# Performance work log

Hardware: AMD Instinct MI355X
Metric: run time of the kernel (lower is better)

The kernel has to match this reference:

```python
import jax, jax.numpy as jnp
import numpy as np

N_NODES = 100000
N_EDGES = 1600000


def setup_inputs() -> dict:
    key = jax.random.key(0)
    ks = jax.random.split(key, 5)
    x = jax.random.normal(ks[0], (N_NODES, 128), dtype=jnp.float32)
    edge_index = jax.random.randint(ks[1], (2, N_EDGES), 0, N_NODES, dtype=jnp.int64)
    edge_weight = jnp.ones((N_EDGES,), dtype=jnp.float32)
    W1 = jax.random.normal(ks[2], (128, 128), dtype=jnp.float32) * (1.0 / np.sqrt(128))
    b1 = jnp.zeros((128,), dtype=jnp.float32)
    W2 = jax.random.normal(ks[3], (128, 64), dtype=jnp.float32) * (1.0 / np.sqrt(128))
    b2 = jnp.zeros((64,), dtype=jnp.float32)
    return {"x": x, "edge_index": edge_index, "edge_weight": edge_weight,
            "W1": W1, "b1": b1, "W2": W2, "b2": b2}


def _gcn_conv(x, rows, cols, W, b, n_nodes):
    # GCNConv(normalize=True), unit edge weights (forward overwrites weights with ones)
    h = x @ W                                             # [N, out]
    ones_w = jnp.ones(rows.shape[0], dtype=x.dtype)
    deg = jax.ops.segment_sum(ones_w, cols, num_segments=n_nodes)   # in-degree at targets
    dinv = jnp.where(deg > 0, deg ** -0.5, 0.0)
    norm = dinv[rows] * dinv[cols]                        # [E+N]
    msg = h[rows] * norm[:, None]                         # gather + scale, memory-bound
    out = jax.ops.segment_sum(msg, cols, num_segments=n_nodes)
    return out + b


def reference(x, edge_index, edge_weight, W1, b1, W2, b2):
    n = x.shape[0]
    loop = jnp.arange(n, dtype=edge_index.dtype)
    rows = jnp.concatenate([edge_index[0], loop])         # self-loops (PyG default)
    cols = jnp.concatenate([edge_index[1], loop])
    h = jax.nn.relu(_gcn_conv(x, rows, cols, W1, b1, n))
    logits = _gcn_conv(h, rows, cols, W2, b2, n)
    return logits
```

## Files before the change

kernel.cpp:

```cpp
#include <hip/hip_runtime.h>
#include <hip/hip_fp16.h>


constexpr int NN = 100000;
constexpr int NE = 1600000;
constexpr int BSH = 7;
constexpr int NB = (NN + 127) >> BSH;
constexpr int NBLK = 256;
constexpr int EPB = NE / NBLK;
constexpr int TSTR = 784;

typedef _Float16 f16x8 __attribute__((ext_vector_type(8)));
typedef float f32x4 __attribute__((ext_vector_type(4)));

__global__ __launch_bounds__(256) void k_hist(const int* __restrict__ cols,
                                              int* __restrict__ table) {
  __shared__ int cnt[NB];
  for (int i = threadIdx.x; i < NB; i += 256) cnt[i] = 0;
  __syncthreads();
  int base = blockIdx.x * EPB;
  for (int i = threadIdx.x; i < EPB; i += 256)
    atomicAdd(&cnt[cols[base + i] >> BSH], 1);
  __syncthreads();
  for (int i = threadIdx.x; i < NB; i += 256)
    table[blockIdx.x * TSTR + i] = cnt[i];
}

__global__ __launch_bounds__(256) void k_scanT(const int* __restrict__ table,
                                               int* __restrict__ startOff,
                                               int* __restrict__ btot) {
  __shared__ int s[256];
  int b = blockIdx.x, t = threadIdx.x;
  int v = table[t * TSTR + b];
  s[t] = v;
  __syncthreads();
  for (int off = 1; off < 256; off <<= 1) {
    int tmp = (t >= off) ? s[t - off] : 0;
    __syncthreads();
    s[t] += tmp;
    __syncthreads();
  }
  startOff[t * TSTR + b] = s[t] - v;
  if (t == 255) btot[b] = s[t];
}

__global__ __launch_bounds__(256) void k_scanBkt(const int* __restrict__ btot,
                                                 int* __restrict__ bucketBase) {
  __shared__ int s[256];
  int t = threadIdx.x;
  int base = t * 4;
  int d0 = (base + 0 < NB) ? btot[base + 0] : 0;
  int d1 = (base + 1 < NB) ? btot[base + 1] : 0;
  int d2 = (base + 2 < NB) ? btot[base + 2] : 0;
  int d3 = (base + 3 < NB) ? btot[base + 3] : 0;
  int tsum = d0 + d1 + d2 + d3;
  s[t] = tsum;
  __syncthreads();
  for (int off = 1; off < 256; off <<= 1) {
    int tmp = (t >= off) ? s[t - off] : 0;
    __syncthreads();
    s[t] += tmp;
    __syncthreads();
  }
  int ex = s[t] - tsum;
  if (base + 0 < NB) bucketBase[base + 0] = ex;
  if (base + 1 < NB) bucketBase[base + 1] = ex + d0;
  if (base + 2 < NB) bucketBase[base + 2] = ex + d0 + d1;
  if (base + 3 < NB) bucketBase[base + 3] = ex + d0 + d1 + d2;
}

__global__ __launch_bounds__(256) void k_scat(const int* __restrict__ rows,
                                              const int* __restrict__ cols,
                                              const int* __restrict__ startOff,
                                              const int* __restrict__ bucketBase,
                                              unsigned* __restrict__ binned) {
  __shared__ int scnt[NB];
  int blk = blockIdx.x;
  for (int i = threadIdx.x; i < NB; i += 256)
    scnt[i] = bucketBase[i] + startOff[blk * TSTR + i];
  __syncthreads();
  int base = blk * EPB;
  for (int i = threadIdx.x; i < EPB; i += 256) {
    int c = cols[base + i];
    int r = rows[base + i];
    int pos = atomicAdd(&scnt[c >> BSH], 1);
    binned[pos] = ((unsigned)r << BSH) | (unsigned)(c & 127);
  }
}

__global__ __launch_bounds__(256) void k_fillb(const unsigned* __restrict__ binned,
                                               const int* __restrict__ bucketBase,
                                               const int* __restrict__ btot,
                                               int* __restrict__ rowptr,
                                               int* __restrict__ deg,
                                               float* __restrict__ dinv,
                                               int* __restrict__ srcIdx,
                                               const float4* __restrict__ x4,
                                               float2* __restrict__ y8) {
  __shared__ int cnt[128];
  __shared__ int sc[128];
  __shared__ int rp[128];
  __shared__ float sdv[128];
  int b = blockIdx.x;
  int nb0 = b << BSH;
  int nn = min(128, NN - nb0);
  int tid = threadIdx.x;
  if (tid < 128) cnt[tid] = 0;
  __syncthreads();
  int ebeg = bucketBase[b];
  int eend = ebeg + btot[b];
  for (int p = ebeg + tid; p < eend; p += 256)
    atomicAdd(&cnt[binned[p] & 127], 1);
  __syncthreads();
  int v = (tid < 128) ? cnt[tid] : 0;
  if (tid < 128) sc[tid] = v;
  __syncthreads();
  for (int off = 1; off < 128; off <<= 1) {
    int tmp = (tid < 128 && tid >= off) ? sc[tid - off] : 0;
    __syncthreads();
    if (tid < 128) sc[tid] += tmp;
    __syncthreads();
  }
  if (tid < 128) {
    int ex = sc[tid] - v;
    rp[tid] = ebeg + ex;
    float dv = rsqrtf((float)v + 1.0f);
    sdv[tid] = dv;
    if (tid < nn) {
      rowptr[nb0 + tid] = ebeg + ex;
      deg[nb0 + tid] = v;
      dinv[nb0 + tid] = dv;
    }
    cnt[tid] = 0;
  }
  __syncthreads();
  for (int p = ebeg + tid; p < eend; p += 256) {
    unsigned pk = binned[p];
    int cl = pk & 127;
    int local = atomicAdd(&cnt[cl], 1);
    srcIdx[rp[cl] + local] = (int)(pk >> BSH);
  }
  int tot = nn << 5;
  const float4* xb = x4 + ((size_t)nb0 << 5);
  float2* yb = y8 + ((size_t)nb0 << 5);
  for (int i = tid; i < tot; i += 256) {
    float s = sdv[i >> 5];
    float4 vv = xb[i];
    union { __half2 h[2]; float2 f; } u;
    u.h[0] = __floats2half2_rn(vv.x * s, vv.y * s);
    u.h[1] = __floats2half2_rn(vv.z * s, vv.w * s);
    yb[i] = u.f;
  }
}

__global__ __launch_bounds__(256) void k_wt(const float* __restrict__ W1,
                                            const float* __restrict__ W2,
                                            __half* __restrict__ Wt1,
                                            __half* __restrict__ Wt2) {
  int i = blockIdx.x * 256 + threadIdx.x;
  if (i < 16384) {
    int k = i >> 7, n = i & 127;
    Wt1[n * 128 + k] = __float2half(W1[i]);
  } else {
    int j = i - 16384;
    int k = j >> 6, n = j & 63;
    Wt2[n * 128 + k] = __float2half(W2[j]);
  }
}

__global__ __launch_bounds__(256, 8) void k_fused(
    const __half* __restrict__ y, const int* __restrict__ rowptr,
    const int* __restrict__ deg, const int* __restrict__ srcIdx,
    const float* __restrict__ dinv, const __half* __restrict__ Wt1,
    const float* __restrict__ b1, const __half* __restrict__ Wt2,
    __half* __restrict__ z) {
  __shared__ __align__(16) __half sA[16][136];
  __shared__ __align__(16) __half sB[16][136];
  const int w = threadIdx.x >> 6, l = threadIdx.x & 63;
  const int blk0 = blockIdx.x * 16;
  const int quad = l >> 4, m = l & 15;

  for (int i = 0; i < 4; ++i) {
    const int lr = w * 4 + i;
    const int node = blk0 + lr;
    const int d = deg[node];
    const int ptr = rowptr[node];
    float acc[8];
#pragma unroll
    for (int j = 0; j < 8; j++) acc[j] = 0.0f;
    for (int base = 0; base < d; base += 64) {
      int cnt = min(64, d - base);
      int my = (l < cnt) ? srcIdx[ptr + base + l] : 0;
      int k = 0;
      for (; k + 16 <= cnt; k += 16) {
        int s0 = __shfl(my, k + quad);
        int s1 = __shfl(my, k + 4 + quad);
        int s2 = __shfl(my, k + 8 + quad);
        int s3 = __shfl(my, k + 12 + quad);
        f16x8 v0 = *reinterpret_cast<const f16x8*>(y + (size_t)s0 * 128 + m * 8);
        f16x8 v1 = *reinterpret_cast<const f16x8*>(y + (size_t)s1 * 128 + m * 8);
        f16x8 v2 = *reinterpret_cast<const f16x8*>(y + (size_t)s2 * 128 + m * 8);
        f16x8 v3 = *reinterpret_cast<const f16x8*>(y + (size_t)s3 * 128 + m * 8);
#pragma unroll
        for (int j = 0; j < 8; j++) acc[j] += (float)v0[j];
#pragma unroll
        for (int j = 0; j < 8; j++) acc[j] += (float)v1[j];
#pragma unroll
        for (int j = 0; j < 8; j++) acc[j] += (float)v2[j];
#pragma unroll
        for (int j = 0; j < 8; j++) acc[j] += (float)v3[j];
      }
      for (; k + 8 <= cnt; k += 8) {
        int s0 = __shfl(my, k + quad);
        int s1 = __shfl(my, k + 4 + quad);
        f16x8 v0 = *reinterpret_cast<const f16x8*>(y + (size_t)s0 * 128 + m * 8);
        f16x8 v1 = *reinterpret_cast<const f16x8*>(y + (size_t)s1 * 128 + m * 8);
#pragma unroll
        for (int j = 0; j < 8; j++) acc[j] += (float)v0[j];
#pragma unroll
        for (int j = 0; j < 8; j++) acc[j] += (float)v1[j];
      }
      for (; k < cnt; k += 4) {
        int idx = k + quad;
        bool valid = idx < cnt;
        int s0 = __shfl(my, valid ? idx : 0);
        f16x8 v0 = *reinterpret_cast<const f16x8*>(y + (size_t)s0 * 128 + m * 8);
        if (valid) {
#pragma unroll
          for (int j = 0; j < 8; j++) acc[j] += (float)v0[j];
        }
      }
    }
#pragma unroll
    for (int j = 0; j < 8; j++) acc[j] += __shfl_xor(acc[j], 16);
#pragma unroll
    for (int j = 0; j < 8; j++) acc[j] += __shfl_xor(acc[j], 32);
    if (quad == 0) {
      f16x8 sv = *reinterpret_cast<const f16x8*>(y + (size_t)node * 128 + m * 8);
      float scn = dinv[node];
      f16x8 o;
#pragma unroll
      for (int j = 0; j < 8; j++)
        o[j] = (_Float16)((acc[j] + (float)sv[j]) * scn);
      *reinterpret_cast<f16x8*>(&sA[lr][m * 8]) = o;
    }
  }
  __syncthreads();

  f16x8 afrag[4];
#pragma unroll
  for (int kk = 0; kk < 4; kk++)
    afrag[kk] = *reinterpret_cast<const f16x8*>(&sA[m][kk * 32 + quad * 8]);
  f32x4 acc1[2];
#pragma unroll
  for (int t = 0; t < 2; t++) {
    float bv = b1[(w * 2 + t) * 16 + m];
    acc1[t] = (f32x4){bv, bv, bv, bv};
  }
#pragma unroll
  for (int kk = 0; kk < 4; kk++) {
#pragma unroll
    for (int t = 0; t < 2; t++) {
      f16x8 b = *reinterpret_cast<const f16x8*>(
          Wt1 + (size_t)((w * 2 + t) * 16 + m) * 128 + kk * 32 + quad * 8);
      acc1[t] = __builtin_amdgcn_mfma_f32_16x16x32_f16(afrag[kk], b, acc1[t], 0, 0, 0);
    }
  }
#pragma unroll
  for (int t = 0; t < 2; t++)
#pragma unroll
    for (int i = 0; i < 4; i++)
      sB[quad * 4 + i][(w * 2 + t) * 16 + m] =
          __float2half(fmaxf(acc1[t][i], 0.0f));
  __syncthreads();

  f16x8 hfrag[4];
#pragma unroll
  for (int kk = 0; kk < 4; kk++)
    hfrag[kk] = *reinterpret_cast<const f16x8*>(&sB[m][kk * 32 + quad * 8]);
  f32x4 acc2 = (f32x4){0.f, 0.f, 0.f, 0.f};
#pragma unroll
  for (int kk = 0; kk < 4; kk++) {
    f16x8 b = *reinterpret_cast<const f16x8*>(
        Wt2 + (size_t)(w * 16 + m) * 128 + kk * 32 + quad * 8);
    acc2 = __builtin_amdgcn_mfma_f32_16x16x32_f16(hfrag[kk], b, acc2, 0, 0, 0);
  }
  float rs[4];
#pragma unroll
  for (int i = 0; i < 4; i++) rs[i] = dinv[blk0 + quad * 4 + i];
#pragma unroll
  for (int i = 0; i < 4; i++)
    sA[quad * 4 + i][w * 16 + m] = __float2half(acc2[i] * rs[i]);
  __syncthreads();

  if (threadIdx.x < 128) {
    int r = threadIdx.x >> 3, cc = threadIdx.x & 7;
    *reinterpret_cast<float4*>(z + (size_t)(blk0 + r) * 64 + cc * 8) =
        *reinterpret_cast<const float4*>(&sA[r][cc * 8]);
  }
}

__global__ __launch_bounds__(256) void k_gath2(const __half* __restrict__ z,
                                               const int* __restrict__ rowptr,
                                               const int* __restrict__ deg,
                                               const int* __restrict__ srcIdx,
                                               const float* __restrict__ dinv,
                                               const float* __restrict__ b2,
                                               float* __restrict__ out) {
  int node = blockIdx.x * 4 + (threadIdx.x >> 6);
  if (node >= NN) return;
  int lane = threadIdx.x & 63;
  int g = lane >> 3;
  int c = lane & 7;
  int d = deg[node];
  int p = rowptr[node];
  size_t coff = (size_t)c * 8;
  float acc[8];
#pragma unroll
  for (int i = 0; i < 8; i++) acc[i] = 0.0f;

  for (int base = 0; base < d; base += 64) {
    int cnt = min(64, d - base);
    int my = (lane < cnt) ? srcIdx[p + base + lane] : 0;
    int k = 0;
    for (; k + 16 <= cnt; k += 16) {
      int s0 = __shfl(my, k + g);
      int s1 = __shfl(my, k + 8 + g);
      f16x8 v0 = *reinterpret_cast<const f16x8*>(z + (size_t)s0 * 64 + coff);
      f16x8 v1 = *reinterpret_cast<const f16x8*>(z + (size_t)s1 * 64 + coff);
#pragma unroll
      for (int i = 0; i < 8; i++) acc[i] += (float)v0[i];
#pragma unroll
      for (int i = 0; i < 8; i++) acc[i] += (float)v1[i];
    }
    for (; k < cnt; k += 8) {
      int idx = k + g;
      bool valid = idx < cnt;
      int s0 = __shfl(my, valid ? idx : 0);
      f16x8 v0 = *reinterpret_cast<const f16x8*>(z + (size_t)s0 * 64 + coff);
      if (valid) {
#pragma unroll
        for (int i = 0; i < 8; i++) acc[i] += (float)v0[i];
      }
    }
  }
#pragma unroll
  for (int i = 0; i < 8; i++) acc[i] += __shfl_xor(acc[i], 8);
#pragma unroll
  for (int i = 0; i < 8; i++) acc[i] += __shfl_xor(acc[i], 16);
#pragma unroll
  for (int i = 0; i < 8; i++) acc[i] += __shfl_xor(acc[i], 32);
  if (g == 0) {
    f16x8 sv = *reinterpret_cast<const f16x8*>(z + (size_t)node * 64 + coff);
    float s = dinv[node];
    const float4* b4 = reinterpret_cast<const float4*>(b2);
    float4 bv0 = b4[2 * c], bv1 = b4[2 * c + 1];
    float4 o0, o1;
    o0.x = (acc[0] + (float)sv[0]) * s + bv0.x;
    o0.y = (acc[1] + (float)sv[1]) * s + bv0.y;
    o0.z = (acc[2] + (float)sv[2]) * s + bv0.z;
    o0.w = (acc[3] + (float)sv[3]) * s + bv0.w;
    o1.x = (acc[4] + (float)sv[4]) * s + bv1.x;
    o1.y = (acc[5] + (float)sv[5]) * s + bv1.y;
    o1.z = (acc[6] + (float)sv[6]) * s + bv1.z;
    o1.w = (acc[7] + (float)sv[7]) * s + bv1.w;
    float4* op = reinterpret_cast<float4*>(out + (size_t)node * 64 + coff);
    op[0] = o0;
    op[1] = o1;
  }
}

extern "C" void kernel_launch(void* const* d_in, const int* in_sizes, int n_in,
                              void* d_out, int out_size, void* d_ws, size_t ws_size,
                              hipStream_t stream) {
  const float* x  = (const float*)d_in[0];
  const int*   ei = (const int*)d_in[1];
  const int* rows = ei;
  const int* cols = ei + NE;
  const float* W1 = (const float*)d_in[3];
  const float* b1 = (const float*)d_in[4];
  const float* W2 = (const float*)d_in[5];
  const float* b2 = (const float*)d_in[6];
  float* out = (float*)d_out;

  char* base = (char*)d_ws;
  constexpr size_t MB = 1 << 20;
  int*      deg       = (int*)(base + 0 * MB);
  int*      rowptr    = (int*)(base + 1 * MB);
  float*    dinv      = (float*)(base + 2 * MB);
  int*      btot      = (int*)(base + 3 * MB);
  int*      bucketBase= (int*)(base + 3 * MB + 16 * 1024);
  __half*   Wt1       = (__half*)(base + 3 * MB + 64 * 1024);
  __half*   Wt2       = (__half*)(base + 3 * MB + 128 * 1024);
  int*      table     = (int*)(base + 4 * MB);
  int*      startOff  = (int*)(base + 5 * MB);
  unsigned* binned    = (unsigned*)(base + 6 * MB);
  int*      srcIdx    = (int*)(base + 13 * MB);
  __half*   y         = (__half*)(base + 20 * MB);
  __half*   z         = (__half*)(base + 46 * MB);

  k_wt<<<96, 256, 0, stream>>>(W1, W2, Wt1, Wt2);
  k_hist<<<NBLK, 256, 0, stream>>>(cols, table);
  k_scanT<<<NB, 256, 0, stream>>>(table, startOff, btot);
  k_scanBkt<<<1, 256, 0, stream>>>(btot, bucketBase);
  k_scat<<<NBLK, 256, 0, stream>>>(rows, cols, startOff, bucketBase, binned);
  k_fillb<<<NB, 256, 0, stream>>>(binned, bucketBase, btot, rowptr, deg, dinv,
                                  srcIdx, (const float4*)x, (float2*)y);
  k_fused<<<NN / 16, 256, 0, stream>>>(y, rowptr, deg, srcIdx, dinv,
                                       Wt1, b1, Wt2, z);
  k_gath2<<<(NN + 3) / 4, 256, 0, stream>>>(z, rowptr, deg, srcIdx, dinv, b2, out);
}
```

Before: 302.2 us.

## Merge all GCN stages into one persistent kernel with grid barriers

Replaces the eight separate kernel launches (histogram, scans, scatter, CSR fill, fused layer-1 GEMM, layer-2 gather) with a single persistent cooperative-style kernel. Grid-wide atomic barriers separate the phases, and the final gather uses an atomic work counter for dynamic load balancing. The aim is to remove launch overhead and inter-kernel gaps. In exchange it adds spin-wait barrier cost, relies on every block being co-resident for correctness, and leaves fewer blocks resident for the memory-bound gather phases.

```diff
diff --git a/kernel.cpp b/kernel.cpp
--- a/kernel.cpp
+++ b/kernel.cpp
@@ -9,372 +9,405 @@
 constexpr int NBLK = 256;
 constexpr int EPB = NE / NBLK;
 constexpr int TSTR = 784;
+constexpr int NTILE = NN / 16;
+constexpr int NG4 = NN / 4;
 
 typedef _Float16 f16x8 __attribute__((ext_vector_type(8)));
 typedef float f32x4 __attribute__((ext_vector_type(4)));
 
-__global__ __launch_bounds__(256) void k_hist(const int* __restrict__ cols,
-                                              int* __restrict__ table) {
-  __shared__ int cnt[NB];
-  for (int i = threadIdx.x; i < NB; i += 256) cnt[i] = 0;
+__device__ __forceinline__ void gsync(int* cnt, int* gen, int& local) {
   __syncthreads();
-  int base = blockIdx.x * EPB;
-  for (int i = threadIdx.x; i < EPB; i += 256)
-    atomicAdd(&cnt[cols[base + i] >> BSH], 1);
+  if (threadIdx.x == 0) {
+    int a = __hip_atomic_fetch_add(cnt, 1, __ATOMIC_ACQ_REL,
+                                   __HIP_MEMORY_SCOPE_AGENT);
+    if (a == (int)gridDim.x - 1) {
+      __hip_atomic_store(cnt, 0, __ATOMIC_RELAXED, __HIP_MEMORY_SCOPE_AGENT);
+      __hip_atomic_fetch_add(gen, 1, __ATOMIC_ACQ_REL,
+                             __HIP_MEMORY_SCOPE_AGENT);
+    } else {
+      while (__hip_atomic_load(gen, __ATOMIC_RELAXED,
+                               __HIP_MEMORY_SCOPE_SYSTEM) < local + 1)
+        __builtin_amdgcn_s_sleep(2);
+      (void)__hip_atomic_load(gen, __ATOMIC_ACQUIRE, __HIP_MEMORY_SCOPE_AGENT);
+    }
+  }
+  local++;
   __syncthreads();
-  for (int i = threadIdx.x; i < NB; i += 256)
-    table[blockIdx.x * TSTR + i] = cnt[i];
 }
 
-__global__ __launch_bounds__(256) void k_scanT(const int* __restrict__ table,
-                                               int* __restrict__ startOff,
-                                               int* __restrict__ btot) {
-  __shared__ int s[256];
-  int b = blockIdx.x, t = threadIdx.x;
-  int v = table[t * TSTR + b];
-  s[t] = v;
-  __syncthreads();
-  for (int off = 1; off < 256; off <<= 1) {
-    int tmp = (t >= off) ? s[t - off] : 0;
-    __syncthreads();
-    s[t] += tmp;
-    __syncthreads();
-  }
-  startOff[t * TSTR + b] = s[t] - v;
-  if (t == 255) btot[b] = s[t];
-}
-
-__global__ __launch_bounds__(256) void k_scanBkt(const int* __restrict__ btot,
-                                                 int* __restrict__ bucketBase) {
-  __shared__ int s[256];
-  int t = threadIdx.x;
-  int base = t * 4;
-  int d0 = (base + 0 < NB) ? btot[base + 0] : 0;
-  int d1 = (base + 1 < NB) ? btot[base + 1] : 0;
-  int d2 = (base + 2 < NB) ? btot[base + 2] : 0;
-  int d3 = (base + 3 < NB) ? btot[base + 3] : 0;
-  int tsum = d0 + d1 + d2 + d3;
-  s[t] = tsum;
-  __syncthreads();
-  for (int off = 1; off < 256; off <<= 1) {
-    int tmp = (t >= off) ? s[t - off] : 0;
-    __syncthreads();
-    s[t] += tmp;
-    __syncthreads();
-  }
-  int ex = s[t] - tsum;
-  if (base + 0 < NB) bucketBase[base + 0] = ex;
-  if (base + 1 < NB) bucketBase[base + 1] = ex + d0;
-  if (base + 2 < NB) bucketBase[base + 2] = ex + d0 + d1;
-  if (base + 3 < NB) bucketBase[base + 3] = ex + d0 + d1 + d2;
-}
-
-__global__ __launch_bounds__(256) void k_scat(const int* __restrict__ rows,
-                                              const int* __restrict__ cols,
-                                              const int* __restrict__ startOff,
-                                              const int* __restrict__ bucketBase,
-                                              unsigned* __restrict__ binned) {
-  __shared__ int scnt[NB];
-  int blk = blockIdx.x;
-  for (int i = threadIdx.x; i < NB; i += 256)
-    scnt[i] = bucketBase[i] + startOff[blk * TSTR + i];
-  __syncthreads();
-  int base = blk * EPB;
-  for (int i = threadIdx.x; i < EPB; i += 256) {
-    int c = cols[base + i];
-    int r = rows[base + i];
-    int pos = atomicAdd(&scnt[c >> BSH], 1);
-    binned[pos] = ((unsigned)r << BSH) | (unsigned)(c & 127);
-  }
-}
-
-__global__ __launch_bounds__(256) void k_fillb(const unsigned* __restrict__ binned,
-                                               const int* __restrict__ bucketBase,
-                                               const int* __restrict__ btot,
-                                               int* __restrict__ rowptr,
-                                               int* __restrict__ deg,
-                                               float* __restrict__ dinv,
-                                               int* __restrict__ srcIdx,
-                                               const float4* __restrict__ x4,
-                                               float2* __restrict__ y8) {
-  __shared__ int cnt[128];
-  __shared__ int sc[128];
-  __shared__ int rp[128];
-  __shared__ float sdv[128];
-  int b = blockIdx.x;
-  int nb0 = b << BSH;
-  int nn = min(128, NN - nb0);
-  int tid = threadIdx.x;
-  if (tid < 128) cnt[tid] = 0;
-  __syncthreads();
-  int ebeg = bucketBase[b];
-  int eend = ebeg + btot[b];
-  for (int p = ebeg + tid; p < eend; p += 256)
-    atomicAdd(&cnt[binned[p] & 127], 1);
-  __syncthreads();
-  int v = (tid < 128) ? cnt[tid] : 0;
-  if (tid < 128) sc[tid] = v;
-  __syncthreads();
-  for (int off = 1; off < 128; off <<= 1) {
-    int tmp = (tid < 128 && tid >= off) ? sc[tid - off] : 0;
-    __syncthreads();
-    if (tid < 128) sc[tid] += tmp;
-    __syncthreads();
-  }
-  if (tid < 128) {
-    int ex = sc[tid] - v;
-    rp[tid] = ebeg + ex;
-    float dv = rsqrtf((float)v + 1.0f);
-    sdv[tid] = dv;
-    if (tid < nn) {
-      rowptr[nb0 + tid] = ebeg + ex;
-      deg[nb0 + tid] = v;
-      dinv[nb0 + tid] = dv;
-    }
-    cnt[tid] = 0;
-  }
-  __syncthreads();
-  for (int p = ebeg + tid; p < eend; p += 256) {
-    unsigned pk = binned[p];
-    int cl = pk & 127;
-    int local = atomicAdd(&cnt[cl], 1);
-    srcIdx[rp[cl] + local] = (int)(pk >> BSH);
-  }
-  int tot = nn << 5;
-  const float4* xb = x4 + ((size_t)nb0 << 5);
-  float2* yb = y8 + ((size_t)nb0 << 5);
-  for (int i = tid; i < tot; i += 256) {
-    float s = sdv[i >> 5];
-    float4 vv = xb[i];
-    union { __half2 h[2]; float2 f; } u;
-    u.h[0] = __floats2half2_rn(vv.x * s, vv.y * s);
-    u.h[1] = __floats2half2_rn(vv.z * s, vv.w * s);
-    yb[i] = u.f;
-  }
-}
-
-__global__ __launch_bounds__(256) void k_wt(const float* __restrict__ W1,
-                                            const float* __restrict__ W2,
-                                            __half* __restrict__ Wt1,
-                                            __half* __restrict__ Wt2) {
-  int i = blockIdx.x * 256 + threadIdx.x;
-  if (i < 16384) {
-    int k = i >> 7, n = i & 127;
-    Wt1[n * 128 + k] = __float2half(W1[i]);
-  } else {
-    int j = i - 16384;
-    int k = j >> 6, n = j & 63;
-    Wt2[n * 128 + k] = __float2half(W2[j]);
-  }
-}
-
-__global__ __launch_bounds__(256, 8) void k_fused(
-    const __half* __restrict__ y, const int* __restrict__ rowptr,
-    const int* __restrict__ deg, const int* __restrict__ srcIdx,
-    const float* __restrict__ dinv, const __half* __restrict__ Wt1,
-    const float* __restrict__ b1, const __half* __restrict__ Wt2,
-    __half* __restrict__ z) {
-  __shared__ __align__(16) __half sA[16][136];
-  __shared__ __align__(16) __half sB[16][136];
-  const int w = threadIdx.x >> 6, l = threadIdx.x & 63;
-  const int blk0 = blockIdx.x * 16;
-  const int quad = l >> 4, m = l & 15;
-
-  for (int i = 0; i < 4; ++i) {
-    const int lr = w * 4 + i;
-    const int node = blk0 + lr;
-    const int d = deg[node];
-    const int ptr = rowptr[node];
-    float acc[8];
-#pragma unroll
-    for (int j = 0; j < 8; j++) acc[j] = 0.0f;
-    for (int base = 0; base < d; base += 64) {
-      int cnt = min(64, d - base);
-      int my = (l < cnt) ? srcIdx[ptr + base + l] : 0;
-      int k = 0;
-      for (; k + 16 <= cnt; k += 16) {
-        int s0 = __shfl(my, k + quad);
-        int s1 = __shfl(my, k + 4 + quad);
-        int s2 = __shfl(my, k + 8 + quad);
-        int s3 = __shfl(my, k + 12 + quad);
-        f16x8 v0 = *reinterpret_cast<const f16x8*>(y + (size_t)s0 * 128 + m * 8);
-        f16x8 v1 = *reinterpret_cast<const f16x8*>(y + (size_t)s1 * 128 + m * 8);
-        f16x8 v2 = *reinterpret_cast<const f16x8*>(y + (size_t)s2 * 128 + m * 8);
-        f16x8 v3 = *reinterpret_cast<const f16x8*>(y + (size_t)s3 * 128 + m * 8);
-#pragma unroll
-        for (int j = 0; j < 8; j++) acc[j] += (float)v0[j];
-#pragma unroll
-        for (int j = 0; j < 8; j++) acc[j] += (float)v1[j];
-#pragma unroll
-        for (int j = 0; j < 8; j++) acc[j] += (float)v2[j];
-#pragma unroll
-        for (int j = 0; j < 8; j++) acc[j] += (float)v3[j];
+__global__ __launch_bounds__(256, 8) void k_mega(
+    const float4* __restrict__ x4, const int* __restrict__ rows,
+    const int* __restrict__ cols, const float* __restrict__ W1,
+    const float* __restrict__ b1, const float* __restrict__ W2,
+    const float* __restrict__ b2, float* __restrict__ out,
+    int* __restrict__ table, int* __restrict__ startOff,
+    int* __restrict__ btot, int* __restrict__ bucketBase,
+    unsigned* __restrict__ binned, int* __restrict__ rowptr,
+    int* __restrict__ deg, float* __restrict__ dinv,
+    int* __restrict__ srcIdx, __half* __restrict__ Wt1,
+    __half* __restrict__ Wt2, __half* __restrict__ y,
+    __half* __restrict__ z, int* ctl) {
+  __shared__ __align__(16) char smem[8704];
+  __shared__ int sclaim;
+  const int tid = threadIdx.x;
+  const int nb_ = gridDim.x;
+  int* bcnt = ctl + 0;
+  int* bgen = ctl + 1;
+  int local = 0;
+
+  for (int vb = blockIdx.x; vb < NBLK + 96; vb += nb_) {
+    if (vb < NBLK) {
+      int* cnt = (int*)smem;
+      for (int i = tid; i < NB; i += 256) cnt[i] = 0;
+      __syncthreads();
+      int base = vb * EPB;
+      for (int i = tid; i < EPB; i += 256)
+        atomicAdd(&cnt[cols[base + i] >> BSH], 1);
+      __syncthreads();
+      for (int i = tid; i < NB; i += 256) table[vb * TSTR + i] = cnt[i];
+      __syncthreads();
+    } else {
+      int i = (vb - NBLK) * 256 + tid;
+      if (i < 16384) {
+        int k = i >> 7, n = i & 127;
+        Wt1[n * 128 + k] = __float2half(W1[i]);
+      } else {
+        int j = i - 16384;
+        int k = j >> 6, n = j & 63;
+        Wt2[n * 128 + k] = __float2half(W2[j]);
       }
-      for (; k + 8 <= cnt; k += 8) {
-        int s0 = __shfl(my, k + quad);
-        int s1 = __shfl(my, k + 4 + quad);
-        f16x8 v0 = *reinterpret_cast<const f16x8*>(y + (size_t)s0 * 128 + m * 8);
-        f16x8 v1 = *reinterpret_cast<const f16x8*>(y + (size_t)s1 * 128 + m * 8);
-#pragma unroll
-        for (int j = 0; j < 8; j++) acc[j] += (float)v0[j];
-#pragma unroll
-        for (int j = 0; j < 8; j++) acc[j] += (float)v1[j];
+    }
+  }
+  gsync(bcnt, bgen, local);
+
+  for (int vb = blockIdx.x; vb < NB; vb += nb_) {
+    int* s = (int*)smem;
+    int v = table[tid * TSTR + vb];
+    s[tid] = v;
+    __syncthreads();
+    for (int off = 1; off < 256; off <<= 1) {
+      int tmp = (tid >= off) ? s[tid - off] : 0;
+      __syncthreads();
+      s[tid] += tmp;
+      __syncthreads();
+    }
+    startOff[tid * TSTR + vb] = s[tid] - v;
+    if (tid == 255) btot[vb] = s[tid];
+    __syncthreads();
+  }
+  gsync(bcnt, bgen, local);
+
+  if (blockIdx.x < NBLK) {
+    int* bb = (int*)smem;
+    int* s = (int*)(smem + 3200);
+    int* scnt = (int*)(smem + 4352);
+    int base4 = tid * 4;
+    int d0 = (base4 + 0 < NB) ? btot[base4 + 0] : 0;
+    int d1 = (base4 + 1 < NB) ? btot[base4 + 1] : 0;
+    int d2 = (base4 + 2 < NB) ? btot[base4 + 2] : 0;
+    int d3 = (base4 + 3 < NB) ? btot[base4 + 3] : 0;
+    int tsum = d0 + d1 + d2 + d3;
+    s[tid] = tsum;
+    __syncthreads();
+    for (int off = 1; off < 256; off <<= 1) {
+      int tmp = (tid >= off) ? s[tid - off] : 0;
+      __syncthreads();
+      s[tid] += tmp;
+      __syncthreads();
+    }
+    int ex = s[tid] - tsum;
+    if (base4 + 0 < NB) bb[base4 + 0] = ex;
+    if (base4 + 1 < NB) bb[base4 + 1] = ex + d0;
+    if (base4 + 2 < NB) bb[base4 + 2] = ex + d0 + d1;
+    if (base4 + 3 < NB) bb[base4 + 3] = ex + d0 + d1 + d2;
+    __syncthreads();
+    if (blockIdx.x == 0)
+      for (int i = tid; i < NB; i += 256) bucketBase[i] = bb[i];
+    for (int vb = blockIdx.x; vb < NBLK; vb += nb_) {
+      for (int i = tid; i < NB; i += 256)
+        scnt[i] = bb[i] + startOff[vb * TSTR + i];
+      __syncthreads();
+      int base = vb * EPB;
+      for (int i = tid; i < EPB; i += 256) {
+        int c = cols[base + i];
+        int r = rows[base + i];
+        int pos = atomicAdd(&scnt[c >> BSH], 1);
+        binned[pos] = ((unsigned)r << BSH) | (unsigned)(c & 127);
       }
-      for (; k < cnt; k += 4) {
-        int idx = k + quad;
-        bool valid = idx < cnt;
-        int s0 = __shfl(my, valid ? idx : 0);
-        f16x8 v0 = *reinterpret_cast<const f16x8*>(y + (size_t)s0 * 128 + m * 8);
-        if (valid) {
-#pragma unroll
-          for (int j = 0; j < 8; j++) acc[j] += (float)v0[j];
-        }
+      __syncthreads();
+    }
+  }
+  gsync(bcnt, bgen, local);
+
+  for (int vb = blockIdx.x; vb < NB; vb += nb_) {
+    int* cnt = (int*)smem;
+    int* sc = cnt + 128;
+    int* rp = sc + 128;
+    int nb0 = vb << BSH;
+    int nn = min(128, NN - nb0);
+    if (tid < 128) cnt[tid] = 0;
+    __syncthreads();
+    int ebeg = bucketBase[vb];
+    int eend = ebeg + btot[vb];
+    for (int p = ebeg + tid; p < eend; p += 256)
+      atomicAdd(&cnt[binned[p] & 127], 1);
+    __syncthreads();
+    int v = (tid < 128) ? cnt[tid] : 0;
+    if (tid < 128) sc[tid] = v;
+    __syncthreads();
+    for (int off = 1; off < 128; off <<= 1) {
+      int tmp = (tid < 128 && tid >= off) ? sc[tid - off] : 0;
+      __syncthreads();
+      if (tid < 128) sc[tid] += tmp;
+      __syncthreads();
+    }
+    if (tid < 128) {
+      int ex = sc[tid] - v;
+      rp[tid] = ebeg + ex;
+      if (tid < nn) {
+        rowptr[nb0 + tid] = ebeg + ex;
+        deg[nb0 + tid] = v;
+        dinv[nb0 + tid] = rsqrtf((float)v + 1.0f);
       }
-    }
-#pragma unroll
-    for (int j = 0; j < 8; j++) acc[j] += __shfl_xor(acc[j], 16);
-#pragma unroll
-    for (int j = 0; j < 8; j++) acc[j] += __shfl_xor(acc[j], 32);
-    if (quad == 0) {
-      f16x8 sv = *reinterpret_cast<const f16x8*>(y + (size_t)node * 128 + m * 8);
-      float scn = dinv[node];
-      f16x8 o;
-#pragma unroll
-      for (int j = 0; j < 8; j++)
-        o[j] = (_Float16)((acc[j] + (float)sv[j]) * scn);
-      *reinterpret_cast<f16x8*>(&sA[lr][m * 8]) = o;
-    }
-  }
-  __syncthreads();
-
-  f16x8 afrag[4];
-#pragma unroll
-  for (int kk = 0; kk < 4; kk++)
-    afrag[kk] = *reinterpret_cast<const f16x8*>(&sA[m][kk * 32 + quad * 8]);
-  f32x4 acc1[2];
-#pragma unroll
-  for (int t = 0; t < 2; t++) {
-    float bv = b1[(w * 2 + t) * 16 + m];
-    acc1[t] = (f32x4){bv, bv, bv, bv};
-  }
-#pragma unroll
-  for (int kk = 0; kk < 4; kk++) {
-#pragma unroll
-    for (int t = 0; t < 2; t++) {
-      f16x8 b = *reinterpret_cast<const f16x8*>(
-          Wt1 + (size_t)((w * 2 + t) * 16 + m) * 128 + kk * 32 + quad * 8);
-      acc1[t] = __builtin_amdgcn_mfma_f32_16x16x32_f16(afrag[kk], b, acc1[t], 0, 0, 0);
-    }
-  }
-#pragma unroll
-  for (int t = 0; t < 2; t++)
-#pragma unroll
-    for (int i = 0; i < 4; i++)
-      sB[quad * 4 + i][(w * 2 + t) * 16 + m] =
-          __float2half(fmaxf(acc1[t][i], 0.0f));
-  __syncthreads();
-
-  f16x8 hfrag[4];
-#pragma unroll
-  for (int kk = 0; kk < 4; kk++)
-    hfrag[kk] = *reinterpret_cast<const f16x8*>(&sB[m][kk * 32 + quad * 8]);
-  f32x4 acc2 = (f32x4){0.f, 0.f, 0.f, 0.f};
-#pragma unroll
-  for (int kk = 0; kk < 4; kk++) {
-    f16x8 b = *reinterpret_cast<const f16x8*>(
-        Wt2 + (size_t)(w * 16 + m) * 128 + kk * 32 + quad * 8);
-    acc2 = __builtin_amdgcn_mfma_f32_16x16x32_f16(hfrag[kk], b, acc2, 0, 0, 0);
-  }
-  float rs[4];
-#pragma unroll
-  for (int i = 0; i < 4; i++) rs[i] = dinv[blk0 + quad * 4 + i];
-#pragma unroll
-  for (int i = 0; i < 4; i++)
-    sA[quad * 4 + i][w * 16 + m] = __float2half(acc2[i] * rs[i]);
-  __syncthreads();
-
-  if (threadIdx.x < 128) {
-    int r = threadIdx.x >> 3, cc = threadIdx.x & 7;
-    *reinterpret_cast<float4*>(z + (size_t)(blk0 + r) * 64 + cc * 8) =
-        *reinterpret_cast<const float4*>(&sA[r][cc * 8]);
-  }
-}
-
-__global__ __launch_bounds__(256) void k_gath2(const __half* __restrict__ z,
-                                               const int* __restrict__ rowptr,
-                                               const int* __restrict__ deg,
-                                               const int* __restrict__ srcIdx,
-                                               const float* __restrict__ dinv,
-                                               const float* __restrict__ b2,
-                                               float* __restrict__ out) {
-  int node = blockIdx.x * 4 + (threadIdx.x >> 6);
-  if (node >= NN) return;
-  int lane = threadIdx.x & 63;
-  int g = lane >> 3;
-  int c = lane & 7;
-  int d = deg[node];
-  int p = rowptr[node];
-  size_t coff = (size_t)c * 8;
-  float acc[8];
-#pragma unroll
-  for (int i = 0; i < 8; i++) acc[i] = 0.0f;
-
-  for (int base = 0; base < d; base += 64) {
-    int cnt = min(64, d - base);
-    int my = (lane < cnt) ? srcIdx[p + base + lane] : 0;
-    int k = 0;
-    for (; k + 16 <= cnt; k += 16) {
-      int s0 = __shfl(my, k + g);
-      int s1 = __shfl(my, k + 8 + g);
-      f16x8 v0 = *reinterpret_cast<const f16x8*>(z + (size_t)s0 * 64 + coff);
-      f16x8 v1 = *reinterpret_cast<const f16x8*>(z + (size_t)s1 * 64 + coff);
-#pragma unroll
-      for (int i = 0; i < 8; i++) acc[i] += (float)v0[i];
-#pragma unroll
-      for (int i = 0; i < 8; i++) acc[i] += (float)v1[i];
-    }
-    for (; k < cnt; k += 8) {
-      int idx = k + g;
-      bool valid = idx < cnt;
-      int s0 = __shfl(my, valid ? idx : 0);
-      f16x8 v0 = *reinterpret_cast<const f16x8*>(z + (size_t)s0 * 64 + coff);
-      if (valid) {
-#pragma unroll
-        for (int i = 0; i < 8; i++) acc[i] += (float)v0[i];
+      cnt[tid] = 0;
+    }
+    __syncthreads();
+    for (int p = ebeg + tid; p < eend; p += 256) {
+      unsigned pk = binned[p];
+      int cl = pk & 127;
+      int lo = atomicAdd(&cnt[cl], 1);
+      srcIdx[rp[cl] + lo] = (int)(pk >> BSH);
+    }
+    __syncthreads();
+  }
+  gsync(bcnt, bgen, local);
+
+  {
+    float2* y8 = (float2*)y;
+    for (int i = blockIdx.x * 256 + tid; i < NN * 32; i += nb_ * 256) {
+      float sfac = dinv[i >> 5];
+      float4 vv = x4[i];
+      union { __half2 h[2]; float2 f; } u;
+      u.h[0] = __floats2half2_rn(vv.x * sfac, vv.y * sfac);
+      u.h[1] = __floats2half2_rn(vv.z * sfac, vv.w * sfac);
+      y8[i] = u.f;
+    }
+  }
+  gsync(bcnt, bgen, local);
+
+  {
+    __half(*sA)[136] = (__half(*)[136])smem;
+    __half(*sB)[136] = (__half(*)[136])(smem + 4352);
+    const int w = tid >> 6, l = tid & 63;
+    const int quad = l >> 4, m = l & 15;
+    for (;;) {
+      if (tid == 0) sclaim = atomicAdd(ctl + 2, 1);
+      __syncthreads();
+      const int t0 = sclaim * 2;
+      if (t0 >= NTILE) break;
+      const int t1 = (t0 + 2 < NTILE) ? t0 + 2 : NTILE;
+      for (int tile = t0; tile < t1; ++tile) {
+        const int blk0 = tile * 16;
+        for (int i = 0; i < 4; ++i) {
+          const int lr = w * 4 + i;
+          const int node = blk0 + lr;
+          const int d = deg[node];
+          const int ptr = rowptr[node];
+          float acc[8];
+#pragma unroll
+          for (int j = 0; j < 8; j++) acc[j] = 0.0f;
+          for (int base = 0; base < d; base += 64) {
+            int cntv = min(64, d - base);
+            int my = (l < cntv) ? srcIdx[ptr + base + l] : 0;
+            int k = 0;
+            for (; k + 16 <= cntv; k += 16) {
+              int s0 = __shfl(my, k + quad);
+              int s1 = __shfl(my, k + 4 + quad);
+              int s2 = __shfl(my, k + 8 + quad);
+              int s3 = __shfl(my, k + 12 + quad);
+              f16x8 v0 = *(const f16x8*)(y + (size_t)s0 * 128 + m * 8);
+              f16x8 v1 = *(const f16x8*)(y + (size_t)s1 * 128 + m * 8);
+              f16x8 v2 = *(const f16x8*)(y + (size_t)s2 * 128 + m * 8);
+              f16x8 v3 = *(const f16x8*)(y + (size_t)s3 * 128 + m * 8);
+#pragma unroll
+              for (int j = 0; j < 8; j++) acc[j] += (float)v0[j];
+#pragma unroll
+              for (int j = 0; j < 8; j++) acc[j] += (float)v1[j];
+#pragma unroll
+              for (int j = 0; j < 8; j++) acc[j] += (float)v2[j];
+#pragma unroll
+              for (int j = 0; j < 8; j++) acc[j] += (float)v3[j];
+            }
+            for (; k + 8 <= cntv; k += 8) {
+              int s0 = __shfl(my, k + quad);
+              int s1 = __shfl(my, k + 4 + quad);
+              f16x8 v0 = *(const f16x8*)(y + (size_t)s0 * 128 + m * 8);
+              f16x8 v1 = *(const f16x8*)(y + (size_t)s1 * 128 + m * 8);
+#pragma unroll
+              for (int j = 0; j < 8; j++) acc[j] += (float)v0[j];
+#pragma unroll
+              for (int j = 0; j < 8; j++) acc[j] += (float)v1[j];
+            }
+            for (; k < cntv; k += 4) {
+              int idx = k + quad;
+              bool valid = idx < cntv;
+              int s0 = __shfl(my, valid ? idx : 0);
+              f16x8 v0 = *(const f16x8*)(y + (size_t)s0 * 128 + m * 8);
+              if (valid) {
+#pragma unroll
+                for (int j = 0; j < 8; j++) acc[j] += (float)v0[j];
+              }
+            }
+          }
+#pragma unroll
+          for (int j = 0; j < 8; j++) acc[j] += __shfl_xor(acc[j], 16);
+#pragma unroll
+          for (int j = 0; j < 8; j++) acc[j] += __shfl_xor(acc[j], 32);
+          if (quad == 0) {
+            f16x8 sv = *(const f16x8*)(y + (size_t)node * 128 + m * 8);
+            float scn = dinv[node];
+            f16x8 o;
+#pragma unroll
+            for (int j = 0; j < 8; j++)
+              o[j] = (_Float16)((acc[j] + (float)sv[j]) * scn);
+            *(f16x8*)(&sA[lr][m * 8]) = o;
+          }
+        }
+        __syncthreads();
+        f16x8 afrag[4];
+#pragma unroll
+        for (int kk = 0; kk < 4; kk++)
+          afrag[kk] = *(const f16x8*)(&sA[m][kk * 32 + quad * 8]);
+        f32x4 acc1[2];
+#pragma unroll
+        for (int t = 0; t < 2; t++) {
+          float bv = b1[(w * 2 + t) * 16 + m];
+          acc1[t] = (f32x4){bv, bv, bv, bv};
+        }
+#pragma unroll
+        for (int kk = 0; kk < 4; kk++) {
+#pragma unroll
+          for (int t = 0; t < 2; t++) {
+            f16x8 b = *(const f16x8*)(Wt1 + (size_t)((w * 2 + t) * 16 + m) * 128 +
+                                      kk * 32 + quad * 8);
+            acc1[t] =
+                __builtin_amdgcn_mfma_f32_16x16x32_f16(afrag[kk], b, acc1[t], 0, 0, 0);
+          }
+        }
+#pragma unroll
+        for (int t = 0; t < 2; t++)
+#pragma unroll
+          for (int i = 0; i < 4; i++)
+            sB[quad * 4 + i][(w * 2 + t) * 16 + m] =
+                __float2half(fmaxf(acc1[t][i], 0.0f));
+        __syncthreads();
+        f16x8 hfrag[4];
+#pragma unroll
+        for (int kk = 0; kk < 4; kk++)
+          hfrag[kk] = *(const f16x8*)(&sB[m][kk * 32 + quad * 8]);
+        f32x4 acc2 = (f32x4){0.f, 0.f, 0.f, 0.f};
+#pragma unroll
+        for (int kk = 0; kk < 4; kk++) {
+          f16x8 b = *(const f16x8*)(Wt2 + (size_t)(w * 16 + m) * 128 + kk * 32 +
+                                    quad * 8);
+          acc2 = __builtin_amdgcn_mfma_f32_16x16x32_f16(hfrag[kk], b, acc2, 0, 0, 0);
+        }
+        float rs[4];
+#pragma unroll
+        for (int i = 0; i < 4; i++) rs[i] = dinv[blk0 + quad * 4 + i];
+#pragma unroll
+        for (int i = 0; i < 4; i++)
+          sA[quad * 4 + i][w * 16 + m] = __float2half(acc2[i] * rs[i]);
+        __syncthreads();
+        if (tid < 128) {
+          int r = tid >> 3, cc = tid & 7;
+          *(float4*)(z + (size_t)(blk0 + r) * 64 + cc * 8) =
+              *(const float4*)(&sA[r][cc * 8]);
+        }
+        __syncthreads();
       }
     }
   }
-#pragma unroll
-  for (int i = 0; i < 8; i++) acc[i] += __shfl_xor(acc[i], 8);
-#pragma unroll
-  for (int i = 0; i < 8; i++) acc[i] += __shfl_xor(acc[i], 16);
-#pragma unroll
-  for (int i = 0; i < 8; i++) acc[i] += __shfl_xor(acc[i], 32);
-  if (g == 0) {
-    f16x8 sv = *reinterpret_cast<const f16x8*>(z + (size_t)node * 64 + coff);
-    float s = dinv[node];
-    const float4* b4 = reinterpret_cast<const float4*>(b2);
-    float4 bv0 = b4[2 * c], bv1 = b4[2 * c + 1];
-    float4 o0, o1;
-    o0.x = (acc[0] + (float)sv[0]) * s + bv0.x;
-    o0.y = (acc[1] + (float)sv[1]) * s + bv0.y;
-    o0.z = (acc[2] + (float)sv[2]) * s + bv0.z;
-    o0.w = (acc[3] + (float)sv[3]) * s + bv0.w;
-    o1.x = (acc[4] + (float)sv[4]) * s + bv1.x;
-    o1.y = (acc[5] + (float)sv[5]) * s + bv1.y;
-    o1.z = (acc[6] + (float)sv[6]) * s + bv1.z;
-    o1.w = (acc[7] + (float)sv[7]) * s + bv1.w;
-    float4* op = reinterpret_cast<float4*>(out + (size_t)node * 64 + coff);
-    op[0] = o0;
-    op[1] = o1;
+  gsync(bcnt, bgen, local);
+
+  {
+    const int lane = tid & 63;
+    const int g = lane >> 3;
+    const int c = lane & 7;
+    const size_t coff = (size_t)c * 8;
+    for (;;) {
+      if (tid == 0) sclaim = atomicAdd(ctl + 3, 1);
+      __syncthreads();
+      const int g0 = sclaim * 4;
+      if (g0 >= NG4) break;
+      const int g1 = (g0 + 4 < NG4) ? g0 + 4 : NG4;
+      for (int gg = g0; gg < g1; ++gg) {
+        int node = gg * 4 + (tid >> 6);
+        int d = deg[node];
+        int p = rowptr[node];
+        float acc[8];
+#pragma unroll
+        for (int i = 0; i < 8; i++) acc[i] = 0.0f;
+        for (int base = 0; base < d; base += 64) {
+          int cnt = min(64, d - base);
+          int my = (lane < cnt) ? srcIdx[p + base + lane] : 0;
+          int k = 0;
+          for (; k + 16 <= cnt; k += 16) {
+            int s0 = __shfl(my, k + g);
+            int s1 = __shfl(my, k + 8 + g);
+            f16x8 v0 = *(const f16x8*)(z + (size_t)s0 * 64 + coff);
+            f16x8 v1 = *(const f16x8*)(z + (size_t)s1 * 64 + coff);
+#pragma unroll
+            for (int i = 0; i < 8; i++) acc[i] += (float)v0[i];
+#pragma unroll
+            for (int i = 0; i < 8; i++) acc[i] += (float)v1[i];
+          }
+          for (; k < cnt; k += 8) {
+            int idx = k + g;
+            bool valid = idx < cnt;
+            int s0 = __shfl(my, valid ? idx : 0);
+            f16x8 v0 = *(const f16x8*)(z + (size_t)s0 * 64 + coff);
+            if (valid) {
+#pragma unroll
+              for (int i = 0; i < 8; i++) acc[i] += (float)v0[i];
+            }
+          }
+        }
+#pragma unroll
+        for (int i = 0; i < 8; i++) acc[i] += __shfl_xor(acc[i], 8);
+#pragma unroll
+        for (int i = 0; i < 8; i++) acc[i] += __shfl_xor(acc[i], 16);
+#pragma unroll
+        for (int i = 0; i < 8; i++) acc[i] += __shfl_xor(acc[i], 32);
+        if (g == 0) {
+          f16x8 sv = *(const f16x8*)(z + (size_t)node * 64 + coff);
+          float s = dinv[node];
+          const float4* b4 = (const float4*)b2;
+          float4 bv0 = b4[2 * c], bv1 = b4[2 * c + 1];
+          float4 o0, o1;
+          o0.x = (acc[0] + (float)sv[0]) * s + bv0.x;
+          o0.y = (acc[1] + (float)sv[1]) * s + bv0.y;
+          o0.z = (acc[2] + (float)sv[2]) * s + bv0.z;
+          o0.w = (acc[3] + (float)sv[3]) * s + bv0.w;
+          o1.x = (acc[4] + (float)sv[4]) * s + bv1.x;
+          o1.y = (acc[5] + (float)sv[5]) * s + bv1.y;
+          o1.z = (acc[6] + (float)sv[6]) * s + bv1.z;
+          o1.w = (acc[7] + (float)sv[7]) * s + bv1.w;
+          float4* op = (float4*)(out + (size_t)node * 64 + coff);
+          op[0] = o0;
+          op[1] = o1;
+        }
+      }
+      __syncthreads();
+    }
   }
 }
 
 extern "C" void kernel_launch(void* const* d_in, const int* in_sizes, int n_in,
                               void* d_out, int out_size, void* d_ws, size_t ws_size,
                               hipStream_t stream) {
-  const float* x  = (const float*)d_in[0];
-  const int*   ei = (const int*)d_in[1];
+  const float* x = (const float*)d_in[0];
+  const int* ei = (const int*)d_in[1];
   const int* rows = ei;
   const int* cols = ei + NE;
   const float* W1 = (const float*)d_in[3];
@@ -385,28 +418,35 @@
 
   char* base = (char*)d_ws;
   constexpr size_t MB = 1 << 20;
-  int*      deg       = (int*)(base + 0 * MB);
-  int*      rowptr    = (int*)(base + 1 * MB);
-  float*    dinv      = (float*)(base + 2 * MB);
-  int*      btot      = (int*)(base + 3 * MB);
-  int*      bucketBase= (int*)(base + 3 * MB + 16 * 1024);
-  __half*   Wt1       = (__half*)(base + 3 * MB + 64 * 1024);
-  __half*   Wt2       = (__half*)(base + 3 * MB + 128 * 1024);
-  int*      table     = (int*)(base + 4 * MB);
-  int*      startOff  = (int*)(base + 5 * MB);
-  unsigned* binned    = (unsigned*)(base + 6 * MB);
-  int*      srcIdx    = (int*)(base + 13 * MB);
-  __half*   y         = (__half*)(base + 20 * MB);
-  __half*   z         = (__half*)(base + 46 * MB);
-
-  k_wt<<<96, 256, 0, stream>>>(W1, W2, Wt1, Wt2);
-  k_hist<<<NBLK, 256, 0, stream>>>(cols, table);
-  k_scanT<<<NB, 256, 0, stream>>>(table, startOff, btot);
-  k_scanBkt<<<1, 256, 0, stream>>>(btot, bucketBase);
-  k_scat<<<NBLK, 256, 0, stream>>>(rows, cols, startOff, bucketBase, binned);
-  k_fillb<<<NB, 256, 0, stream>>>(binned, bucketBase, btot, rowptr, deg, dinv,
-                                  srcIdx, (const float4*)x, (float2*)y);
-  k_fused<<<NN / 16, 256, 0, stream>>>(y, rowptr, deg, srcIdx, dinv,
-                                       Wt1, b1, Wt2, z);
-  k_gath2<<<(NN + 3) / 4, 256, 0, stream>>>(z, rowptr, deg, srcIdx, dinv, b2, out);
+  int* deg = (int*)(base + 0 * MB);
+  int* rowptr = (int*)(base + 1 * MB);
+  float* dinv = (float*)(base + 2 * MB);
+  int* btot = (int*)(base + 3 * MB);
+  int* bucketBase = (int*)(base + 3 * MB + 16 * 1024);
+  __half* Wt1 = (__half*)(base + 3 * MB + 64 * 1024);
+  __half* Wt2 = (__half*)(base + 3 * MB + 128 * 1024);
+  int* ctl = (int*)(base + 3 * MB + 512 * 1024);
+  int* table = (int*)(base + 4 * MB);
+  int* startOff = (int*)(base + 5 * MB);
+  unsigned* binned = (unsigned*)(base + 6 * MB);
+  int* srcIdx = (int*)(base + 13 * MB);
+  __half* y = (__half*)(base + 20 * MB);
+  __half* z = (__half*)(base + 46 * MB);
+
+  hipMemsetAsync(ctl, 0, 16, stream);
+
+  static int nblk = 0;
+  if (nblk == 0) {
+    int b = 0;
+    if (hipOccupancyMaxActiveBlocksPerMultiprocessor(&b, k_mega, 256, 0) !=
+            hipSuccess ||
+        b < 1)
+      b = 4;
+    if (b > 8) b = 8;
+    nblk = b * 256;
+  }
+
+  k_mega<<<nblk, 256, 0, stream>>>(
+      (const float4*)x, rows, cols, W1, b1, W2, b2, out, table, startOff, btot,
+      bucketBase, binned, rowptr, deg, dinv, srcIdx, Wt1, Wt2, y, z, ctl);
 }
```

Measured after the change: 979.5 us. 224% more time.
